# Performance work log

Measured on AMD Instinct MI355X. Metric: run time of the kernel, lower is better.

Reference implementation:

```python
import jax, jax.numpy as jnp
import numpy as np

IN = 128; HID = 128; OUT = 128; HEADS = 3; T1 = 0.2; T2 = 0.2
B = 512; L = 32; V = 100000; NMETA = 5


def _corr_full(s, t):
    # s, t: (B, L, E, N). Full cross-correlation along last axis.
    # Matches F.conv1d(hs, ht, groups=BLE, padding=N-1): out[k] = sum_m s[k+m-(N-1)] * t[m]
    N = s.shape[-1]
    sp = jnp.pad(s, ((0, 0), (0, 0), (0, 0), (N - 1, N - 1)))
    out = jnp.stack([(sp[..., k:k + N] * t).sum(-1) for k in range(2 * N - 1)], axis=-1)
    return jnp.swapaxes(out, -1, -2)  # (B, L, 2N-1, E)


def _node_att(h, Wt, Ws, Wc):
    # h: (B, L, P, E); Wt/Ws/Wc: (HEADS, E, HID)
    Bh, Lh, P, E = h.shape
    H = h.reshape(Bh * Lh, P, E)
    hi = jnp.einsum('ne,heo->hno', H[:, 0], Wt)                 # target-node projection
    logits = jnp.einsum('npe,heo,hno->hnp', H, Ws, hi) / T1     # (heads, BL, P)
    alpha = jax.nn.softmax(logits, axis=-1)                     # softmax over path positions
    Z = jnp.einsum('hnp,npe,heo->no', alpha, H, Wc) / HEADS     # mean over heads
    return Z.reshape(Bh, Lh, -1)


def _forward(emb_user, emb_item, emb_attr1, emb_attr2, emb_attr3, Wt, Ws, Wc,
             pw1, pb1, pw2, fw1, fb1, fw2, fb2,
             UI, IU, UIUI, IUIU, UIAI1, IAIU1, UIAI2, IAIU2, UIAI3, IAIU3):
    src = emb_user[UI[:, 0, 0]]
    tgt = emb_item[IU[:, 0, 0]]
    ui = jnp.stack([emb_user[UI[..., 0]], emb_item[UI[..., 1]]], axis=3)
    iu = jnp.stack([emb_item[IU[..., 0]], emb_user[IU[..., 1]]], axis=3)

    def p4(tabs, idx):
        return jnp.stack([tabs[k][idx[..., k]] for k in range(4)], axis=3)

    uiui = p4([emb_user, emb_item, emb_user, emb_item], UIUI)
    iuiu = p4([emb_item, emb_user, emb_item, emb_user], IUIU)
    uiai1 = p4([emb_user, emb_item, emb_attr1, emb_item], UIAI1)
    iaiu1 = p4([emb_item, emb_attr1, emb_item, emb_user], IAIU1)
    uiai2 = p4([emb_user, emb_item, emb_attr2, emb_item], UIAI2)
    iaiu2 = p4([emb_item, emb_attr2, emb_item, emb_user], IAIU2)
    uiai3 = p4([emb_user, emb_item, emb_attr3, emb_item], UIAI3)
    iaiu3 = p4([emb_item, emb_attr3, emb_item, emb_user], IAIU3)

    user_feats = [ui, uiui, uiai1, uiai2, uiai3]
    item_feats = [iu, iuiu, iaiu1, iaiu2, iaiu3]
    Hs = [_node_att(_corr_full(uf, itf), Wt[m], Ws[m], Wc[m])
          for m, (uf, itf) in enumerate(zip(user_feats, item_feats))]
    Z = jnp.stack(Hs, 1)                        # (B, 5, L, HID)
    z = Z.reshape(Z.shape[0], -1, HID)          # (B, 5L, HID)
    w = jnp.tanh(z @ pw1 + pb1) @ pw2 / T2      # (B, 5L, 1)
    beta = jax.nn.softmax(w, axis=1)
    path_out = (beta * z).sum(1)                # (B, HID)
    x = jnp.concatenate([src, tgt, path_out], axis=1)
    x = jax.nn.relu(x @ fw1 + fb1)              # dropout in eval mode -> identity
    return jax.nn.sigmoid(x @ fw2 + fb2)        # (B, 1)


def setup_inputs() -> dict:
    key = jax.random.key(0)
    ks = jax.random.split(key, 24)

    def idx(k, n):
        return jax.random.randint(k, (B, L, n), 0, V, dtype=jnp.int32)

    d = {
        'UI': idx(ks[0], 2), 'IU': idx(ks[1], 2),
        'UIUI': idx(ks[2], 4), 'IUIU': idx(ks[3], 4),
        'UIAI1': idx(ks[4], 4), 'IAIU1': idx(ks[5], 4),
        'UIAI2': idx(ks[6], 4), 'IAIU2': idx(ks[7], 4),
        'UIAI3': idx(ks[8], 4), 'IAIU3': idx(ks[9], 4),
    }

    def emb(k):
        t = jax.random.normal(k, (V + 1, IN), jnp.float32) * 0.05
        return t.at[0].set(0.0)  # padding_idx=0

    d['emb_user'] = emb(ks[10]); d['emb_item'] = emb(ks[11])
    d['emb_attr1'] = emb(ks[12]); d['emb_attr2'] = emb(ks[13]); d['emb_attr3'] = emb(ks[14])
    s = (2.0 / (IN + HID)) ** 0.5  # xavier scale
    d['Wt'] = jax.random.normal(ks[15], (NMETA, HEADS, IN, HID), jnp.float32) * s
    d['Ws'] = jax.random.normal(ks[16], (NMETA, HEADS, IN, HID), jnp.float32) * s
    d['Wc'] = jax.random.normal(ks[17], (NMETA, HEADS, IN, HID), jnp.float32) * s
    d['pw1'] = jax.random.normal(ks[18], (HID, HID), jnp.float32) * s
    d['pb1'] = jnp.zeros((HID,), jnp.float32)
    d['pw2'] = jax.random.normal(ks[19], (HID, 1), jnp.float32) * s
    d['fw1'] = jax.random.normal(ks[20], (3 * HID, OUT), jnp.float32) * 0.02
    d['fb1'] = jnp.zeros((OUT,), jnp.float32)
    d['fw2'] = jax.random.normal(ks[21], (OUT, 1), jnp.float32) * 0.02
    d['fb2'] = jnp.zeros((1,), jnp.float32)
    return d


def reference(UI, IU, UIUI, IUIU, UIAI1, IAIU1, UIAI2, IAIU2, UIAI3, IAIU3,
              emb_user, emb_item, emb_attr1, emb_attr2, emb_attr3,
              Wt, Ws, Wc, pw1, pb1, pw2, fw1, fb1, fw2, fb2):
    return _forward(emb_user, emb_item, emb_attr1, emb_attr2, emb_attr3, Wt, Ws, Wc,
                    pw1, pb1, pw2, fw1, fb1, fw2, fb2,
                    UI, IU, UIUI, IUIU, UIAI1, IAIU1, UIAI2, IAIU2, UIAI3, IAIU3)
```

## Files before the change

kernel.cpp:

```cpp
#include <hip/hip_runtime.h>
#include <hip/hip_bf16.h>
#include <cstdint>
#include <cstddef>


typedef __hip_bfloat16 bf16;
typedef __attribute__((ext_vector_type(8))) short  bfrag;
typedef __attribute__((ext_vector_type(4))) float  ffrag;

#define NNODES 16384

__device__ __forceinline__ float bflo(uint32_t u) { return __uint_as_float(u << 16); }
__device__ __forceinline__ float bfhi(uint32_t u) { return __uint_as_float(u & 0xffff0000u); }
__device__ __forceinline__ uint16_t f2bfu(float x) {
  bf16 h = __float2bfloat16(x);
  return *(uint16_t*)&h;
}
__device__ __forceinline__ uint32_t pk2(float lo, float hi) {
  return (uint32_t)f2bfu(lo) | ((uint32_t)f2bfu(hi) << 16);
}

__global__ __launch_bounds__(256) void build_BmatT(
    const float* __restrict__ Ws, const float* __restrict__ Wt,
    bf16* __restrict__ BmT)
{
  int mh = blockIdx.x >> 4;
  int g  = blockIdx.x & 15;
  int m = mh / 3, h = mh % 3;
  const float* ws = Ws + (size_t)mh * 16384;
  const float* wt = Wt + (size_t)mh * 16384;
  int tid = threadIdx.x;
  int e = tid & 127, half = tid >> 7;
  __shared__ float wtl[2][128];
  for (int ep0 = g * 8; ep0 < g * 8 + 8; ep0 += 2) {
    int ep = ep0 + half;
    wtl[half][e] = wt[ep * 128 + e];
    __syncthreads();
    float acc = 0.f;
    #pragma unroll 4
    for (int o = 0; o < 128; ++o) acc += ws[e * 128 + o] * wtl[half][o];
    BmT[((size_t)(m * 384 + h * 128 + e)) * 128 + ep] = __float2bfloat16(acc);
    __syncthreads();
  }
}

__global__ __launch_bounds__(256) void conv_WcT(
    const float* __restrict__ Wc, bf16* __restrict__ WcT)
{
  int idx = blockIdx.x * 256 + threadIdx.x;
  int he = idx % 384, mo = idx / 384;
  int m = mo >> 7, o = mo & 127;
  WcT[idx] = __float2bfloat16(Wc[((size_t)m * 384 + he) * 128 + o]);
}

__global__ __launch_bounds__(256) void conv_pw1T(
    const float* __restrict__ pw1, bf16* __restrict__ pw1T)
{
  int idx = blockIdx.x * 256 + threadIdx.x;
  int o = idx >> 7, k = idx & 127;
  pw1T[idx] = __float2bfloat16(pw1[(size_t)k * 128 + o]);
}

template <int P>
__device__ __forceinline__ void metapath_body(
    char* smem,
    const float* __restrict__ Tu0, const float* __restrict__ Tu1,
    const float* __restrict__ Tu2, const float* __restrict__ Tu3,
    const float* __restrict__ Tt0, const float* __restrict__ Tt1,
    const float* __restrict__ Tt2, const float* __restrict__ Tt3,
    const int* __restrict__ idxU, const int* __restrict__ idxT,
    const bf16* __restrict__ BmT,
    const bf16* __restrict__ WcT,
    bf16* __restrict__ Zall, int m, int tile)
{
  constexpr int PP = 2 * P - 1;
  constexpr int NS = PP * 136;
  constexpr int NPAIR = 3 * PP;
  bf16* Hs = (bf16*)smem;
  bf16* Ss = Hs + 16 * NS;

  int tid = threadIdx.x;
  int lane = tid & 63, wid = tid >> 6;
  int l15 = lane & 15, l4 = lane >> 4;
  int n0 = tile * 16;

  {
    const float* TU[4] = {Tu0, Tu1, Tu2, Tu3};
    const float* TT[4] = {Tt0, Tt1, Tt2, Tt3};
    int e = tid & 127;
    float su[4][P], st[4][P];
    #pragma unroll
    for (int g = 0; g < 4; ++g) {
      int n = n0 + g * 4 + (tid >> 7);
      #pragma unroll
      for (int p = 0; p < P; ++p) {
        su[g][p] = TU[p][(size_t)idxU[n * P + p] * 128 + e];
        st[g][p] = TT[p][(size_t)idxT[n * P + p] * 128 + e];
      }
    }
    #pragma unroll
    for (int g = 0; g < 4; ++g) {
      int ln = g * 4 + (tid >> 7);
      bf16* Hn = &Hs[ln * NS + e];
      #pragma unroll
      for (int k = 0; k < PP; ++k) {
        float acc = 0.f;
        #pragma unroll
        for (int i = 0; i < P; ++i) {
          int j = k + i - (P - 1);
          if (j >= 0 && j < P) acc += su[g][j] * st[g][i];
        }
        Hn[k * 136] = __float2bfloat16(acc);
      }
    }
  }
  __syncthreads();

  {
    bfrag a[4];
    #pragma unroll
    for (int kk = 0; kk < 4; ++kk)
      a[kk] = *(const bfrag*)&Hs[l15 * NS + kk * 32 + 8 * l4];
    #pragma unroll
    for (int f = 0; f < 3; ++f) {
      int col = wid * 48 + f * 16 + l15;
      ffrag acc = {0.f, 0.f, 0.f, 0.f};
      #pragma unroll
      for (int kk = 0; kk < 4; ++kk) {
        bfrag b = *(const bfrag*)&BmT[(size_t)col * 128 + kk * 32 + 8 * l4];
        acc = __builtin_amdgcn_mfma_f32_16x16x32_bf16(a[kk], b, acc, 0, 0, 0);
      }
      #pragma unroll
      for (int r = 0; r < 4; ++r) {
        int node = 4 * l4 + r;
        Ss[node * 392 + col] = __float2bfloat16(acc[r]);
      }
    }
  }
  __syncthreads();

  {
    int node = tid >> 5, q = tid & 31;
    int h = q / PP, p = q - h * PP;
    float alpha_mine = 0.f;
    float lg = -1e30f;
    if (q < NPAIR) {
      const uint2* hrow = (const uint2*)&Hs[node * NS + p * 136];
      const uint2* srow = (const uint2*)&Ss[node * 392 + h * 128];
      float acc[4] = {0.f, 0.f, 0.f, 0.f};
      int rot = h * 10;
      #pragma unroll
      for (int ii = 0; ii < 32; ++ii) {
        int iu = (ii + rot) & 31;
        uint2 hv = hrow[iu], sv = srow[iu];
        float t = bflo(hv.x) * bflo(sv.x) + bfhi(hv.x) * bfhi(sv.x)
                + bflo(hv.y) * bflo(sv.y) + bfhi(hv.y) * bfhi(sv.y);
        acc[ii & 3] += t;
      }
      lg = (acc[0] + acc[1] + acc[2] + acc[3]) * 5.0f;
    }
    int base = (lane & 32) + h * PP;
    float mx = lg;
    #pragma unroll
    for (int d = 1; d < PP; ++d) {
      int pd = p + d; if (pd >= PP) pd -= PP;
      mx = fmaxf(mx, __shfl(lg, base + pd, 64));
    }
    float ex = __expf(lg - mx);
    float sm = ex;
    #pragma unroll
    for (int d = 1; d < PP; ++d) {
      int pd = p + d; if (pd >= PP) pd -= PP;
      sm += __shfl(ex, base + pd, 64);
    }
    alpha_mine = ex / sm;

    int hb = lane & 32;
    #pragma unroll
    for (int c = 0; c < 6; ++c) {
      int o2 = q * 6 + c;
      int h2 = o2 >> 6, e2 = (o2 & 63) * 2;
      float a0 = 0.f, a1 = 0.f;
      #pragma unroll
      for (int pp = 0; pp < PP; ++pp) {
        float al = __shfl(alpha_mine, hb + h2 * PP + pp, 64);
        uint32_t hv = *(const uint32_t*)&Hs[node * NS + pp * 136 + e2];
        a0 += al * bflo(hv);
        a1 += al * bfhi(hv);
      }
      *(uint32_t*)&Ss[node * 392 + h2 * 128 + e2] = pk2(a0, a1);
    }
  }
  __syncthreads();

  {
    bfrag a[12];
    #pragma unroll
    for (int kk = 0; kk < 12; ++kk)
      a[kk] = *(const bfrag*)&Ss[l15 * 392 + kk * 32 + 8 * l4];
    int col = wid * 16 + l15;
    ffrag acc = {0.f, 0.f, 0.f, 0.f};
    #pragma unroll
    for (int kk = 0; kk < 12; ++kk) {
      bfrag b = *(const bfrag*)&WcT[(size_t)col * 384 + kk * 32 + 8 * l4];
      acc = __builtin_amdgcn_mfma_f32_16x16x32_bf16(a[kk], b, acc, 0, 0, 0);
    }
    #pragma unroll
    for (int r = 0; r < 4; ++r) {
      int gn = n0 + 4 * l4 + r;
      int crow = (((gn >> 5) * 5 + m) << 5) + (gn & 31);
      Zall[(size_t)crow * 128 + col] = __float2bfloat16(acc[r] * (1.0f / 3.0f));
    }
  }
}

__global__ __launch_bounds__(512) void fused_all(
    const float* __restrict__ emb_user, const float* __restrict__ emb_item,
    const float* __restrict__ emb_a1, const float* __restrict__ emb_a2,
    const float* __restrict__ emb_a3,
    const int* __restrict__ UI,    const int* __restrict__ IU,
    const int* __restrict__ UIUI,  const int* __restrict__ IUIU,
    const int* __restrict__ UIAI1, const int* __restrict__ IAIU1,
    const int* __restrict__ UIAI2, const int* __restrict__ IAIU2,
    const int* __restrict__ UIAI3, const int* __restrict__ IAIU3,
    const bf16* __restrict__ BmT, const bf16* __restrict__ WcT,
    bf16* __restrict__ Zall)
{
  extern __shared__ char smem[];
  int bid = blockIdx.x;
  int m = bid >> 10, tile = bid & 1023;
  if (m == 0) {
    metapath_body<2>(smem, emb_user, emb_item, nullptr, nullptr,
                     emb_item, emb_user, nullptr, nullptr,
                     UI, IU, BmT, WcT, Zall, 0, tile);
  } else {
    const float* u2 = (m == 1) ? emb_user : (m == 2) ? emb_a1
                    : (m == 3) ? emb_a2 : emb_a3;
    const int* iu_ = (m == 1) ? UIUI : (m == 2) ? UIAI1
                   : (m == 3) ? UIAI2 : UIAI3;
    const int* it_ = (m == 1) ? IUIU : (m == 2) ? IAIU1
                   : (m == 3) ? IAIU2 : IAIU3;
    metapath_body<4>(smem, emb_user, emb_item, u2, emb_item,
                     emb_item, u2, emb_item, emb_user,
                     iu_, it_,
                     BmT + (size_t)m * 49152, WcT + (size_t)m * 49152,
                     Zall, m, tile);
  }
}

__global__ __launch_bounds__(512) void fused_tail(
    const bf16* __restrict__ Zall,
    const bf16* __restrict__ pw1T,
    const float* __restrict__ pb1, const float* __restrict__ pw2,
    const int* __restrict__ UI, const int* __restrict__ IU,
    const float* __restrict__ emb_user, const float* __restrict__ emb_item,
    const float* __restrict__ fw1, const float* __restrict__ fb1,
    const float* __restrict__ fw2, const float* __restrict__ fb2,
    float* __restrict__ out)
{
  __shared__ bf16 Zs[160 * 136];
  __shared__ float wrow[160];
  __shared__ float ph[4][128];
  __shared__ float xs[384];
  __shared__ float sred[16];
  __shared__ float yred[2];

  int b = blockIdx.x, tid = threadIdx.x;
  int lane = tid & 63, wid = tid >> 6;
  int l15 = lane & 15, l4 = lane >> 4;

  {
    const float4* src = (const float4*)(Zall + (size_t)b * 160 * 128);
    float4 v[5];
    #pragma unroll
    for (int i = 0; i < 5; ++i) v[i] = src[i * 512 + tid];
    #pragma unroll
    for (int i = 0; i < 5; ++i) {
      int idx = i * 512 + tid;
      int row = idx >> 4, c8 = idx & 15;
      *(float4*)&Zs[row * 136 + c8 * 8] = v[i];
    }
  }
  __syncthreads();

  for (int rf = wid; rf < 10; rf += 8) {
    bfrag a[4];
    #pragma unroll
    for (int kk = 0; kk < 4; ++kk)
      a[kk] = *(const bfrag*)&Zs[(rf * 16 + l15) * 136 + kk * 32 + 8 * l4];
    float part[4] = {0.f, 0.f, 0.f, 0.f};
    #pragma unroll
    for (int f = 0; f < 8; ++f) {
      int col = f * 16 + l15;
      ffrag acc = {0.f, 0.f, 0.f, 0.f};
      #pragma unroll
      for (int kk = 0; kk < 4; ++kk) {
        bfrag bv = *(const bfrag*)&pw1T[(size_t)col * 128 + kk * 32 + 8 * l4];
        acc = __builtin_amdgcn_mfma_f32_16x16x32_bf16(a[kk], bv, acc, 0, 0, 0);
      }
      float bias = pb1[col], w2 = pw2[col];
      #pragma unroll
      for (int r = 0; r < 4; ++r) part[r] += tanhf(acc[r] + bias) * w2;
    }
    #pragma unroll
    for (int d = 1; d < 16; d <<= 1) {
      #pragma unroll
      for (int r = 0; r < 4; ++r) part[r] += __shfl_xor(part[r], d);
    }
    if (l15 == 0) {
      #pragma unroll
      for (int r = 0; r < 4; ++r)
        wrow[rf * 16 + 4 * l4 + r] = part[r] * 5.0f;
    }
  }
  __syncthreads();

  {
    float v = (tid < 160) ? wrow[tid] : -1e30f;
    #pragma unroll
    for (int off = 32; off; off >>= 1) v = fmaxf(v, __shfl_xor(v, off));
    if (lane == 0) sred[wid] = v;
    __syncthreads();
    if (tid < 64) {
      float mval = (lane < 8) ? sred[lane] : -1e30f;
      #pragma unroll
      for (int off = 4; off; off >>= 1) mval = fmaxf(mval, __shfl_xor(mval, off));
      if (lane == 0) sred[8] = mval;
    }
    __syncthreads();
    float mx = sred[8];
    float ev = (tid < 160) ? __expf(wrow[tid] - mx) : 0.f;
    float s = ev;
    #pragma unroll
    for (int off = 32; off; off >>= 1) s += __shfl_xor(s, off);
    if (lane == 0) sred[wid] = s;
    __syncthreads();
    if (tid < 64) {
      float sval = (lane < 8) ? sred[lane] : 0.f;
      #pragma unroll
      for (int off = 4; off; off >>= 1) sval += __shfl_xor(sval, off);
      if (lane == 0) sred[9] = sval;
    }
    __syncthreads();
    if (tid < 160) wrow[tid] = ev / sred[9];
  }
  __syncthreads();

  {
    int e = tid & 127, q = tid >> 7;
    float acc = 0.f;
    #pragma unroll 4
    for (int j = q * 40; j < q * 40 + 40; ++j)
      acc += wrow[j] * __bfloat162float(Zs[j * 136 + e]);
    ph[q][e] = acc;
  }
  __syncthreads();

  {
    int su = UI[b * 64];
    int ti = IU[b * 64];
    if (tid < 128) {
      xs[256 + tid] = ph[0][tid] + ph[1][tid] + ph[2][tid] + ph[3][tid];
    } else if (tid < 256) {
      xs[tid - 128] = emb_user[(size_t)su * 128 + (tid - 128)];
    } else if (tid < 384) {
      xs[tid - 128] = emb_item[(size_t)ti * 128 + (tid - 256)];
    }
  }
  __syncthreads();

  {
    int o = tid & 127, q = tid >> 7;
    float acc = 0.f;
    #pragma unroll 4
    for (int i = q * 96; i < q * 96 + 96; ++i)
      acc += xs[i] * fw1[(size_t)i * 128 + o];
    __syncthreads();
    ph[q][o] = acc;
  }
  __syncthreads();
  if (tid < 128) {
    float y = fmaxf(ph[0][tid] + ph[1][tid] + ph[2][tid] + ph[3][tid] + fb1[tid],
                    0.0f) * fw2[tid];
    #pragma unroll
    for (int off = 32; off; off >>= 1) y += __shfl_down(y, off);
    if ((tid & 63) == 0) yred[tid >> 6] = y;
  }
  __syncthreads();
  if (tid == 0) {
    float s = yred[0] + yred[1] + fb2[0];
    out[b] = 1.0f / (1.0f + expf(-s));
  }
}

extern "C" void kernel_launch(void* const* d_in, const int* in_sizes, int n_in,
                              void* d_out, int out_size, void* d_ws, size_t ws_size,
                              hipStream_t stream)
{
  const int* UI    = (const int*)d_in[0];
  const int* IU    = (const int*)d_in[1];
  const int* UIUI  = (const int*)d_in[2];
  const int* IUIU  = (const int*)d_in[3];
  const int* UIAI1 = (const int*)d_in[4];
  const int* IAIU1 = (const int*)d_in[5];
  const int* UIAI2 = (const int*)d_in[6];
  const int* IAIU2 = (const int*)d_in[7];
  const int* UIAI3 = (const int*)d_in[8];
  const int* IAIU3 = (const int*)d_in[9];
  const float* emb_user = (const float*)d_in[10];
  const float* emb_item = (const float*)d_in[11];
  const float* emb_a1   = (const float*)d_in[12];
  const float* emb_a2   = (const float*)d_in[13];
  const float* emb_a3   = (const float*)d_in[14];
  const float* Wt  = (const float*)d_in[15];
  const float* Ws  = (const float*)d_in[16];
  const float* Wc  = (const float*)d_in[17];
  const float* pw1 = (const float*)d_in[18];
  const float* pb1 = (const float*)d_in[19];
  const float* pw2 = (const float*)d_in[20];
  const float* fw1 = (const float*)d_in[21];
  const float* fb1 = (const float*)d_in[22];
  const float* fw2 = (const float*)d_in[23];
  const float* fb2 = (const float*)d_in[24];
  float* out = (float*)d_out;

  char* wsb = (char*)d_ws;
  bf16*  BmT  = (bf16*)wsb;
  bf16*  WcT  = (bf16*)(wsb + 491520);
  bf16*  pw1T = (bf16*)(wsb + 983040);
  bf16*  Zall = (bf16*)(wsb + 1015808);

  build_BmatT<<<240, 256, 0, stream>>>(Ws, Wt, BmT);
  conv_WcT<<<960, 256, 0, stream>>>(Wc, WcT);
  conv_pw1T<<<64, 256, 0, stream>>>(pw1, pw1T);

  fused_all<<<5120, 512, 43008, stream>>>(
      emb_user, emb_item, emb_a1, emb_a2, emb_a3,
      UI, IU, UIUI, IUIU, UIAI1, IAIU1, UIAI2, IAIU2, UIAI3, IAIU3,
      BmT, WcT, Zall);

  fused_tail<<<512, 512, 0, stream>>>(Zall, pw1T, pb1, pw2,
                                      UI, IU, emb_user, emb_item,
                                      fw1, fb1, fw2, fb2, out);
}
```

Measured before the change: 241.6 us.

## Compute attention logits with MFMA, stage alphas in LDS, merge prep kernels

Replaces the per-thread scalar dot products for attention logits with a bf16 MFMA per wave covering two nodes. The softmax now uses xor-shuffle reductions, and the alphas are written to a small shared-memory buffer. The weighted-sum stage reads those alphas once per node instead of shuffling them, and each thread accumulates all three heads. The three weight-preparation kernels are merged into one launch to cut launch overhead. This adds about 768 bytes of LDS per block and rounds the alphas to bf16, which may slightly change accuracy.

```diff
diff --git a/kernel.cpp b/kernel.cpp
--- a/kernel.cpp
+++ b/kernel.cpp
@@ -12,6 +12,9 @@
 
 __device__ __forceinline__ float bflo(uint32_t u) { return __uint_as_float(u << 16); }
 __device__ __forceinline__ float bfhi(uint32_t u) { return __uint_as_float(u & 0xffff0000u); }
+__device__ __forceinline__ float bfs(short s) {
+  return __uint_as_float(((uint32_t)(unsigned short)s) << 16);
+}
 __device__ __forceinline__ uint16_t f2bfu(float x) {
   bf16 h = __float2bfloat16(x);
   return *(uint16_t*)&h;
@@ -20,45 +23,41 @@
   return (uint32_t)f2bfu(lo) | ((uint32_t)f2bfu(hi) << 16);
 }
 
-__global__ __launch_bounds__(256) void build_BmatT(
+__global__ __launch_bounds__(256) void prep_all(
     const float* __restrict__ Ws, const float* __restrict__ Wt,
-    bf16* __restrict__ BmT)
+    const float* __restrict__ Wc, const float* __restrict__ pw1,
+    bf16* __restrict__ BmT, bf16* __restrict__ WcT, bf16* __restrict__ pw1T)
 {
-  int mh = blockIdx.x >> 4;
-  int g  = blockIdx.x & 15;
-  int m = mh / 3, h = mh % 3;
-  const float* ws = Ws + (size_t)mh * 16384;
-  const float* wt = Wt + (size_t)mh * 16384;
+  int bid = blockIdx.x;
   int tid = threadIdx.x;
-  int e = tid & 127, half = tid >> 7;
-  __shared__ float wtl[2][128];
-  for (int ep0 = g * 8; ep0 < g * 8 + 8; ep0 += 2) {
-    int ep = ep0 + half;
-    wtl[half][e] = wt[ep * 128 + e];
-    __syncthreads();
-    float acc = 0.f;
-    #pragma unroll 4
-    for (int o = 0; o < 128; ++o) acc += ws[e * 128 + o] * wtl[half][o];
-    BmT[((size_t)(m * 384 + h * 128 + e)) * 128 + ep] = __float2bfloat16(acc);
-    __syncthreads();
-  }
-}
-
-__global__ __launch_bounds__(256) void conv_WcT(
-    const float* __restrict__ Wc, bf16* __restrict__ WcT)
-{
-  int idx = blockIdx.x * 256 + threadIdx.x;
-  int he = idx % 384, mo = idx / 384;
-  int m = mo >> 7, o = mo & 127;
-  WcT[idx] = __float2bfloat16(Wc[((size_t)m * 384 + he) * 128 + o]);
-}
-
-__global__ __launch_bounds__(256) void conv_pw1T(
-    const float* __restrict__ pw1, bf16* __restrict__ pw1T)
-{
-  int idx = blockIdx.x * 256 + threadIdx.x;
-  int o = idx >> 7, k = idx & 127;
-  pw1T[idx] = __float2bfloat16(pw1[(size_t)k * 128 + o]);
+  if (bid < 240) {
+    int mh = bid >> 4;
+    int g  = bid & 15;
+    int m = mh / 3, h = mh % 3;
+    const float* ws = Ws + (size_t)mh * 16384;
+    const float* wt = Wt + (size_t)mh * 16384;
+    int e = tid & 127, half = tid >> 7;
+    __shared__ float wtl[2][128];
+    for (int ep0 = g * 8; ep0 < g * 8 + 8; ep0 += 2) {
+      int ep = ep0 + half;
+      wtl[half][e] = wt[ep * 128 + e];
+      __syncthreads();
+      float acc = 0.f;
+      #pragma unroll 4
+      for (int o = 0; o < 128; ++o) acc += ws[e * 128 + o] * wtl[half][o];
+      BmT[((size_t)(m * 384 + h * 128 + e)) * 128 + ep] = __float2bfloat16(acc);
+      __syncthreads();
+    }
+  } else if (bid < 1200) {
+    int idx = (bid - 240) * 256 + tid;
+    int he = idx % 384, mo = idx / 384;
+    int m = mo >> 7, o = mo & 127;
+    WcT[idx] = __float2bfloat16(Wc[((size_t)m * 384 + he) * 128 + o]);
+  } else {
+    int idx = (bid - 1200) * 256 + tid;
+    int o = idx >> 7, k = idx & 127;
+    pw1T[idx] = __float2bfloat16(pw1[(size_t)k * 128 + o]);
+  }
 }
 
 template <int P>
@@ -75,9 +74,9 @@
 {
   constexpr int PP = 2 * P - 1;
   constexpr int NS = PP * 136;
-  constexpr int NPAIR = 3 * PP;
   bf16* Hs = (bf16*)smem;
   bf16* Ss = Hs + 16 * NS;
+  bf16* Al = Ss + 16 * 392;
 
   int tid = threadIdx.x;
   int lane = tid & 63, wid = tid >> 6;
@@ -140,55 +139,70 @@
   __syncthreads();
 
   {
+    int nd0 = wid * 2, nd1 = nd0 + 1;
+    bool hi = (l15 >= 8);
+    int nodeA = hi ? nd1 : nd0;
+    int r15 = hi ? (l15 - 8) : l15;
+    int ah = (r15 < 3) ? r15 : 2;
+    int bp = (r15 < PP) ? r15 : (PP - 1);
+    ffrag lacc = {0.f, 0.f, 0.f, 0.f};
+    #pragma unroll
+    for (int kk = 0; kk < 4; ++kk) {
+      bfrag av = *(const bfrag*)&Ss[nodeA * 392 + ah * 128 + kk * 32 + 8 * l4];
+      bfrag bv = *(const bfrag*)&Hs[nodeA * NS + bp * 136 + kk * 32 + 8 * l4];
+      lacc = __builtin_amdgcn_mfma_f32_16x16x32_bf16(av, bv, lacc, 0, 0, 0);
+    }
+    bool val = ((l4 == 0) && !hi && (l15 < PP)) ||
+               ((l4 == 2) &&  hi && (r15 < PP));
+    float lg0 = val ? lacc[0] * 5.0f : -1e30f;
+    float lg1 = val ? lacc[1] * 5.0f : -1e30f;
+    float lg2 = val ? lacc[2] * 5.0f : -1e30f;
+    float m0 = lg0, m1 = lg1, m2 = lg2;
+    #pragma unroll
+    for (int d = 1; d < 8; d <<= 1) {
+      m0 = fmaxf(m0, __shfl_xor(m0, d));
+      m1 = fmaxf(m1, __shfl_xor(m1, d));
+      m2 = fmaxf(m2, __shfl_xor(m2, d));
+    }
+    float e0 = val ? __expf(lg0 - m0) : 0.f;
+    float e1 = val ? __expf(lg1 - m1) : 0.f;
+    float e2 = val ? __expf(lg2 - m2) : 0.f;
+    float s0 = e0, s1 = e1, s2 = e2;
+    #pragma unroll
+    for (int d = 1; d < 8; d <<= 1) {
+      s0 += __shfl_xor(s0, d);
+      s1 += __shfl_xor(s1, d);
+      s2 += __shfl_xor(s2, d);
+    }
+    if (val) {
+      bf16* Aln = Al + nodeA * 24;
+      Aln[r15]      = __float2bfloat16(e0 / s0);
+      Aln[8 + r15]  = __float2bfloat16(e1 / s1);
+      Aln[16 + r15] = __float2bfloat16(e2 / s2);
+    }
+
     int node = tid >> 5, q = tid & 31;
-    int h = q / PP, p = q - h * PP;
-    float alpha_mine = 0.f;
-    float lg = -1e30f;
-    if (q < NPAIR) {
-      const uint2* hrow = (const uint2*)&Hs[node * NS + p * 136];
-      const uint2* srow = (const uint2*)&Ss[node * 392 + h * 128];
-      float acc[4] = {0.f, 0.f, 0.f, 0.f};
-      int rot = h * 10;
-      #pragma unroll
-      for (int ii = 0; ii < 32; ++ii) {
-        int iu = (ii + rot) & 31;
-        uint2 hv = hrow[iu], sv = srow[iu];
-        float t = bflo(hv.x) * bflo(sv.x) + bfhi(hv.x) * bfhi(sv.x)
-                + bflo(hv.y) * bflo(sv.y) + bfhi(hv.y) * bfhi(sv.y);
-        acc[ii & 3] += t;
-      }
-      lg = (acc[0] + acc[1] + acc[2] + acc[3]) * 5.0f;
-    }
-    int base = (lane & 32) + h * PP;
-    float mx = lg;
-    #pragma unroll
-    for (int d = 1; d < PP; ++d) {
-      int pd = p + d; if (pd >= PP) pd -= PP;
-      mx = fmaxf(mx, __shfl(lg, base + pd, 64));
-    }
-    float ex = __expf(lg - mx);
-    float sm = ex;
-    #pragma unroll
-    for (int d = 1; d < PP; ++d) {
-      int pd = p + d; if (pd >= PP) pd -= PP;
-      sm += __shfl(ex, base + pd, 64);
-    }
-    alpha_mine = ex / sm;
-
-    int hb = lane & 32;
-    #pragma unroll
-    for (int c = 0; c < 6; ++c) {
-      int o2 = q * 6 + c;
-      int h2 = o2 >> 6, e2 = (o2 & 63) * 2;
-      float a0 = 0.f, a1 = 0.f;
+    bfrag al0 = *(const bfrag*)&Al[node * 24];
+    bfrag al1 = *(const bfrag*)&Al[node * 24 + 8];
+    bfrag al2 = *(const bfrag*)&Al[node * 24 + 16];
+    #pragma unroll
+    for (int j = 0; j < 2; ++j) {
+      int e2i = 4 * q + 2 * j;
+      float a00 = 0.f, a01 = 0.f, a10 = 0.f, a11 = 0.f, a20 = 0.f, a21 = 0.f;
       #pragma unroll
       for (int pp = 0; pp < PP; ++pp) {
-        float al = __shfl(alpha_mine, hb + h2 * PP + pp, 64);
-        uint32_t hv = *(const uint32_t*)&Hs[node * NS + pp * 136 + e2];
-        a0 += al * bflo(hv);
-        a1 += al * bfhi(hv);
-      }
-      *(uint32_t*)&Ss[node * 392 + h2 * 128 + e2] = pk2(a0, a1);
+        uint32_t hv = *(const uint32_t*)&Hs[node * NS + pp * 136 + e2i];
+        float lo = bflo(hv), hh = bfhi(hv);
+        float f0 = bfs(al0[pp]);
+        float f1 = bfs(al1[pp]);
+        float f2 = bfs(al2[pp]);
+        a00 += f0 * lo; a01 += f0 * hh;
+        a10 += f1 * lo; a11 += f1 * hh;
+        a20 += f2 * lo; a21 += f2 * hh;
+      }
+      *(uint32_t*)&Ss[node * 392 +       e2i] = pk2(a00, a01);
+      *(uint32_t*)&Ss[node * 392 + 128 + e2i] = pk2(a10, a11);
+      *(uint32_t*)&Ss[node * 392 + 256 + e2i] = pk2(a20, a21);
     }
   }
   __syncthreads();
@@ -430,11 +444,9 @@
   bf16*  pw1T = (bf16*)(wsb + 983040);
   bf16*  Zall = (bf16*)(wsb + 1015808);
 
-  build_BmatT<<<240, 256, 0, stream>>>(Ws, Wt, BmT);
-  conv_WcT<<<960, 256, 0, stream>>>(Wc, WcT);
-  conv_pw1T<<<64, 256, 0, stream>>>(pw1, pw1T);
-
-  fused_all<<<5120, 512, 43008, stream>>>(
+  prep_all<<<1264, 256, 0, stream>>>(Ws, Wt, Wc, pw1, BmT, WcT, pw1T);
+
+  fused_all<<<5120, 512, 43776, stream>>>(
       emb_user, emb_item, emb_a1, emb_a2, emb_a3,
       UI, IU, UIUI, IUIU, UIAI1, IAIU1, UIAI2, IAIU2, UIAI3, IAIU3,
       BmT, WcT, Zall);
```

Measured after the change: 201.8 us. -16.5%, faster.
